# Performance work log

Hardware: AMD Instinct MI355X
Metric: run time of the kernel (lower is better)

## Reference

```python
import jax, jax.numpy as jnp
import numpy as np

N = 16384          # nodes
E_R = 524288       # radial edges (avg degree 32)
E_B = 32768        # bonded edges
N_TYPES = 20       # atom types
CS = 64            # scalar (0e) channels
CV = 32            # vector (1o) channels
EA = 16            # edge_attr_dim
EA_B = EA // 2     # bondedness embedding dim
EA_R = (EA + 1) // 2  # radial basis dim
CUTOFF = 1.5       # effective_radial_cutoff
L = 2              # n_layers
NORM = float(np.sqrt((E_R + E_B) / N))  # ~sqrt(avg degree) message normalization


def setup_inputs() -> dict:
    key = jax.random.key(0)
    ks = jax.random.split(key, 32)
    def rn(i, shape, scale=1.0):
        return jax.random.normal(ks[i], shape, dtype=jnp.float32) * scale
    s_e = 1.0 / np.sqrt(EA)
    inp = {}
    inp["pos"] = rn(0, (N, 3))
    inp["c_noise"] = rn(1, (1,))
    inp["atom_types"] = jax.random.randint(ks[2], (N,), 0, N_TYPES)
    inp["radial_edge_index"] = jax.random.randint(ks[3], (2, E_R), 0, N)
    inp["bonded_edge_index"] = jax.random.randint(ks[4], (2, E_B), 0, N)
    # learned parameters
    inp["atom_tab"] = rn(5, (N_TYPES, CS))
    inp["bond_tab"] = rn(6, (2, EA_B))
    inp["ns0_w"] = rn(7, (CS,), 0.1)
    inp["We0"] = rn(8, (EA, CS), s_e)
    inp["We1"] = rn(9, (EA, CS), s_e)
    inp["Wself0"] = rn(10, (CS, CS), 1.0 / np.sqrt(CS))
    inp["Ws0"] = rn(11, (CS, CS), 1.0 / np.sqrt(CS))
    inp["Wv0"] = rn(12, (CS, CV), 1.0 / np.sqrt(CS))
    inp["ns_w"] = rn(13, (L, CS + CV), 0.1)
    inp["We_ss"] = rn(14, (L, EA, CS), s_e)
    inp["We_vs"] = rn(15, (L, EA, CV), s_e)
    inp["We_sv"] = rn(16, (L, EA, CS), s_e)
    inp["We_vv"] = rn(17, (L, EA, CV), s_e)
    inp["We_vx"] = rn(18, (L, EA, CV), s_e)
    inp["Wmix_s"] = rn(19, (L, CS + CV, CS), 1.0 / np.sqrt(CS + CV))
    inp["Wmix_v"] = rn(20, (L, CS + 2 * CV, CV), 1.0 / np.sqrt(CS + 2 * CV))
    inp["Wself_s"] = rn(21, (L, CS, CS), 1.0 / np.sqrt(CS))
    inp["Wself_v"] = rn(22, (L, CV, CV), 1.0 / np.sqrt(CV))
    inp["skip_w"] = rn(23, (L, 2 * (CS + CV)), 0.1)
    inp["skip_b"] = rn(24, (L, 2 * (CS + CV)), 0.1)
    inp["w_out"] = rn(25, (CV,), 1.0 / np.sqrt(CV))
    inp["gain"] = jnp.asarray(0.5, dtype=jnp.float32)
    return inp


def _radial_basis(d):
    # e3nn soft_one_hot_linspace, basis='gaussian', cutoff=True
    centers = jnp.linspace(0.0, CUTOFF, EA_R + 2)[1:-1]
    step = centers[1] - centers[0]
    diff = (d[:, None] - centers[None, :]) / step
    return jnp.exp(-diff * diff) * 1.12


def reference(pos, c_noise, atom_tab, bond_tab, ns0_w, We0, We1, Wself0, Ws0, Wv0,
              ns_w, We_ss, We_vs, We_sv, We_vv, We_vx, Wmix_s, Wmix_v, Wself_s, Wself_v,
              skip_w, skip_b, w_out, gain, atom_types, radial_edge_index, bonded_edge_index):
    edge_index = jnp.concatenate([radial_edge_index, bonded_edge_index], axis=1)
    bond_mask = jnp.concatenate([jnp.zeros((E_R,), jnp.int32), jnp.ones((E_B,), jnp.int32)])
    src, dst = edge_index[0], edge_index[1]
    edge_vec = pos[src] - pos[dst]                      # [E,3]
    d = jnp.sqrt(jnp.sum(edge_vec * edge_vec, -1) + 1e-12)
    Y1 = jnp.sqrt(3.0) * edge_vec / d[:, None]          # l=1 SH, component norm; Y0 == 1
    edge_attr = jnp.concatenate([bond_tab[bond_mask], _radial_basis(d)], axis=-1)  # [E,EA]

    # atom embedding + initial noise-conditional scaling
    s = atom_tab[atom_types] * (1.0 + c_noise * ns0_w)  # [N,CS]

    # initial projector: scalar-input equivariant conv -> hidden irreps
    w0 = edge_attr @ We0
    w1 = edge_attr @ We1
    s_src = s[src]
    a_s = jax.ops.segment_sum(w0 * s_src, dst, num_segments=N) / NORM
    a_v = jax.ops.segment_sum((w1 * s_src)[:, :, None] * Y1[:, None, :], dst, num_segments=N) / NORM
    s_h = a_s @ Ws0 + s @ Wself0                        # [N,CS]
    v_h = jnp.einsum('nci,cd->ndi', a_v, Wv0)           # [N,CV,3]

    for l in range(L):
        # noise-conditional scaling (per-irrep-channel scalar scale)
        scale = 1.0 + c_noise * ns_w[l]
        ss = s_h * scale[:CS]
        vv = v_h * scale[CS:][None, :, None]
        ss_e = ss[src]
        vv_e = vv[src]
        # edge-attr-conditioned tensor-product weights
        w_ss = edge_attr @ We_ss[l]
        w_vs = edge_attr @ We_vs[l]
        w_sv = edge_attr @ We_sv[l]
        w_vv = edge_attr @ We_vv[l]
        w_vx = edge_attr @ We_vx[l]
        # CG tensor-product messages: 0x0->0, 1x1->0 (dot), 0x1->1, 1x0->1, 1x1->1 (cross)
        vdot = jnp.einsum('eci,ei->ec', vv_e, Y1)
        m_s = jnp.concatenate([w_ss * ss_e, w_vs * vdot], axis=-1)          # [E,CS+CV]
        m_v = jnp.concatenate([
            (w_sv * ss_e)[:, :, None] * Y1[:, None, :],
            w_vv[:, :, None] * vv_e,
            w_vx[:, :, None] * jnp.cross(vv_e, Y1[:, None, :]),
        ], axis=1)                                                          # [E,CS+2CV,3]
        a_s = jax.ops.segment_sum(m_s, dst, num_segments=N) / NORM
        a_v = jax.ops.segment_sum(m_v, dst, num_segments=N) / NORM
        new_s = a_s @ Wmix_s[l] + ss @ Wself_s[l]
        new_v = jnp.einsum('nci,cd->ndi', a_v, Wmix_v[l]) + jnp.einsum('nci,cd->ndi', vv, Wself_v[l])
        # noise-conditional skip connection (gated residual)
        g = jax.nn.sigmoid(skip_b[l] + c_noise * skip_w[l])
        s_h = g[:CS] * s_h + g[CS:2 * CS] * new_s
        g_v = g[2 * CS:]
        v_h = g_v[:CV][None, :, None] * v_h + g_v[CV:][None, :, None] * new_v

    # output head: 1o vectors -> 3D displacement, times output gain
    return jnp.einsum('nci,c->ni', v_h, w_out) * gain
```

## Files before the change

kernel.cpp:

```cpp
#include <hip/hip_runtime.h>
#include <math.h>

#define NA 16384
#define ER 524288
#define EB 32768
#define ET 557056
#define INV_NORM 0.17149858514250882f
#define SQRT3 1.7320508075688772f
#define RB_STEP (1.5f/9.0f)
#define BINS 512
#define DMAX 2.5f
#define INV_H ((float)BINS / DMAX)
#define TBL_ELEMS (2 * BINS * 256)

__device__ __forceinline__ float sigmoidf_(float x) { return 1.f / (1.f + __expf(-x)); }

__device__ __forceinline__ int edge_dst(int e, const int* __restrict__ rad, const int* __restrict__ bon) {
  return (e < ER) ? rad[ER + e] : bon[EB + (e - ER)];
}

__global__ void k_zero(int* __restrict__ count) {
  count[blockIdx.x * 256 + threadIdx.x] = 0;
}

__global__ void k_hist(const int* __restrict__ rad, const int* __restrict__ bon, int* __restrict__ count) {
  int e = blockIdx.x * 256 + threadIdx.x;
  atomicAdd(&count[edge_dst(e, rad, bon)], 1);
}

__global__ void k_scan(int* __restrict__ count, int* __restrict__ offsets) {
  __shared__ int part[256];
  int t = threadIdx.x;
  int base = t * 64;
  int s = 0;
  for (int j = 0; j < 64; ++j) s += count[base + j];
  part[t] = s;
  __syncthreads();
  for (int off = 1; off < 256; off <<= 1) {
    int v = (t >= off) ? part[t - off] : 0;
    __syncthreads();
    part[t] += v;
    __syncthreads();
  }
  int run = part[t] - s;
  for (int j = 0; j < 64; ++j) {
    int c = count[base + j];
    offsets[base + j] = run;
    count[base + j] = run;
    run += c;
  }
  if (t == 255) offsets[NA] = run;
}

__global__ void k_fill(const int* __restrict__ rad, const int* __restrict__ bon,
                       int* __restrict__ cursor, int* __restrict__ sorted) {
  int e = blockIdx.x * 256 + threadIdx.x;
  int d = edge_dst(e, rad, bon);
  int slot = atomicAdd(&cursor[d], 1);
  sorted[slot] = e;
}

__global__ void k_edge_pre(const float* __restrict__ pos,
                           const int* __restrict__ rad, const int* __restrict__ bon,
                           const int* __restrict__ sorted, float* __restrict__ rec8) {
  int idx = blockIdx.x * 256 + threadIdx.x;
  int e = sorted[idx];
  int src, dst, v;
  if (e < ER) { src = rad[e]; dst = rad[ER + e]; v = 0; }
  else        { src = bon[e - ER]; dst = bon[EB + e - ER]; v = 1; }
  float dx = pos[src * 3] - pos[dst * 3];
  float dy = pos[src * 3 + 1] - pos[dst * 3 + 1];
  float dz = pos[src * 3 + 2] - pos[dst * 3 + 2];
  float dist = sqrtf(dx * dx + dy * dy + dz * dz + 1e-12f);
  float inv = 1.f / dist;
  float fq = fminf(dist * INV_H, BINS - 1.001f);
  int q = (int)fq;
  float frac = fq - (float)q;
  int qoff = (v * BINS + q) << 8;
  float* rp = rec8 + (size_t)idx * 8;
  *(float4*)rp = make_float4(__int_as_float(src), SQRT3 * dx * inv, SQRT3 * dy * inv, SQRT3 * dz * inv);
  rp[4] = frac;
  rp[5] = __int_as_float(qoff);
}

__global__ void k_build(const float* __restrict__ We0, const float* __restrict__ We1,
                        const float* __restrict__ We_ss, const float* __restrict__ We_vs,
                        const float* __restrict__ We_sv, const float* __restrict__ We_vv,
                        const float* __restrict__ We_vx, const float* __restrict__ bond_tab,
                        float* __restrict__ tabs) {
  int q = blockIdx.x, t = blockIdx.y, v = blockIdx.z, c = threadIdx.x;
  float d0 = q * (DMAX / BINS), d1 = (q + 1) * (DMAX / BINS);
  float rb0[8], rb1[8];
#pragma unroll
  for (int k = 0; k < 8; ++k) {
    float f0 = (d0 - (k + 1) * RB_STEP) * (1.f / RB_STEP);
    float f1 = (d1 - (k + 1) * RB_STEP) * (1.f / RB_STEP);
    rb0[k] = 1.12f * __expf(-f0 * f0);
    rb1[k] = 1.12f * __expf(-f1 * f1);
  }
  const float* A;
  const float* B;
  int stride, coff;
  bool hasB = true;
  if (t == 0) { A = We0; B = We1; stride = 64; coff = c; }
  else if (t == 1 || t == 3) {
    int l = (t == 3);
    A = We_ss + l * 1024; B = We_sv + l * 1024; stride = 64; coff = c;
  } else {
    int l = (t == 4);
    stride = 32; coff = c & 31;
    if (c < 32) { A = We_vs + l * 512; B = We_vv + l * 512; }
    else        { A = We_vx + l * 512; B = nullptr; hasB = false; }
  }
  float ba = 0, bb = 0, a0 = 0, a1 = 0, b0 = 0, b1 = 0;
#pragma unroll
  for (int k = 0; k < 8; ++k) {
    float bt = bond_tab[v * 8 + k];
    float av_lo = A[k * stride + coff], av_hi = A[(8 + k) * stride + coff];
    ba += bt * av_lo;
    a0 += rb0[k] * av_hi; a1 += rb1[k] * av_hi;
    if (hasB) {
      float bv_lo = B[k * stride + coff], bv_hi = B[(8 + k) * stride + coff];
      bb += bt * bv_lo;
      b0 += rb0[k] * bv_hi; b1 += rb1[k] * bv_hi;
    }
  }
  float* o = tabs + (size_t)t * TBL_ELEMS + (((size_t)v * BINS + q) << 8) + c * 4;
  o[0] = ba + a0; o[1] = a1 - a0; o[2] = bb + b0; o[3] = b1 - b0;
}

__global__ void k_embed(const float* __restrict__ atom_tab, const int* __restrict__ types,
                        const float* __restrict__ ns0_w, const float* __restrict__ cnoise,
                        float* __restrict__ s_feat) {
  int tid = blockIdx.x * 256 + threadIdx.x;
  int n = tid >> 6, c = tid & 63;
  float cn = cnoise[0];
  s_feat[tid] = atom_tab[types[n] * 64 + c] * (1.f + cn * ns0_w[c]);
}

__global__ __launch_bounds__(256, 6) void k_agg0(
    const int* __restrict__ offsets, const float* __restrict__ rec8,
    const float* __restrict__ T0, const float* __restrict__ s_feat,
    float* __restrict__ a_s, float* __restrict__ a_v) {
  int lane = threadIdx.x & 63;
  int n = blockIdx.x * 4 + (threadIdx.x >> 6);
  float acc = 0, a0 = 0, a1 = 0, a2 = 0;
  int beg = __builtin_amdgcn_readfirstlane(offsets[n]);
  int end = __builtin_amdgcn_readfirstlane(offsets[n + 1]);
  if (beg < end) {
    const float* rp0 = rec8 + (size_t)beg * 8;
    float4 rA = *(const float4*)rp0;
    float2 rB = *(const float2*)(rp0 + 4);
    int i1 = beg + (beg + 1 < end ? 1 : 0);
    const float* rp1 = rec8 + (size_t)i1 * 8;
    float4 nA = *(const float4*)rp1;
    float2 nB = *(const float2*)(rp1 + 4);
    float4 t4 = *(const float4*)(T0 + __float_as_int(rB.y) + (lane << 2));
    float sv = s_feat[((size_t)__float_as_int(rA.x) << 6) + lane];
#pragma unroll 2
    for (int idx = beg; idx < end; ++idx) {
      float4 pt4 = *(const float4*)(T0 + __float_as_int(nB.y) + (lane << 2));
      float psv = s_feat[((size_t)__float_as_int(nA.x) << 6) + lane];
      int i2 = (idx + 2 < end) ? idx + 2 : end - 1;
      const float* rp2 = rec8 + (size_t)i2 * 8;
      float4 fA = *(const float4*)rp2;
      float2 fB = *(const float2*)(rp2 + 4);
      float frac = rB.x;
      float w0 = fmaf(frac, t4.y, t4.x);
      float w1 = fmaf(frac, t4.w, t4.z);
      acc += w0 * sv;
      float t = w1 * sv;
      a0 += t * rA.y; a1 += t * rA.z; a2 += t * rA.w;
      rA = nA; rB = nB; nA = fA; nB = fB; t4 = pt4; sv = psv;
    }
  }
  a_s[n * 64 + lane] = acc * INV_NORM;
  *(float4*)(a_v + ((size_t)n << 8) + (lane << 2)) =
      make_float4(a0 * INV_NORM, a1 * INV_NORM, a2 * INV_NORM, 0.f);
}

__global__ __launch_bounds__(256, 6) void k_agg_layer(
    const float* __restrict__ cnoise, const float* __restrict__ nsw,
    const int* __restrict__ offsets, const float* __restrict__ rec8,
    const float* __restrict__ TS, const float* __restrict__ TU,
    const float* __restrict__ sh_in, const float* __restrict__ vh_in,
    float* __restrict__ a_s, float* __restrict__ a_v) {
  int lane = threadIdx.x & 63;
  int n = blockIdx.x * 4 + (threadIdx.x >> 6);
  int vc = lane & 31;
  bool low = lane < 32;
  float cn = cnoise[0];
  float scale_s = 1.f + cn * nsw[lane];
  float scale_v = 1.f + cn * nsw[64 + vc];

  float ms = 0;
  float av0 = 0, av1 = 0, av2 = 0;
  float ms2 = 0;
  float b0 = 0, b1 = 0, b2 = 0;
  int beg = __builtin_amdgcn_readfirstlane(offsets[n]);
  int end = __builtin_amdgcn_readfirstlane(offsets[n + 1]);
  if (beg < end) {
    const float* rp0 = rec8 + (size_t)beg * 8;
    float4 rA = *(const float4*)rp0;
    float2 rB = *(const float2*)(rp0 + 4);
    int i1 = beg + (beg + 1 < end ? 1 : 0);
    const float* rp1 = rec8 + (size_t)i1 * 8;
    float4 nA = *(const float4*)rp1;
    float2 nB = *(const float2*)(rp1 + 4);
    int src0 = __float_as_int(rA.x);
    int qo0 = __float_as_int(rB.y);
    float4 s4 = *(const float4*)(TS + qo0 + (lane << 2));
    float4 u4 = *(const float4*)(TU + qo0 + (lane << 2));
    float ss = sh_in[((size_t)src0 << 6) + lane];
    float4 v4 = *(const float4*)(vh_in + ((size_t)src0 << 7) + (vc << 2));
#pragma unroll 2
    for (int idx = beg; idx < end; ++idx) {
      int nsrc = __float_as_int(nA.x);
      int nqo = __float_as_int(nB.y);
      float4 ps4 = *(const float4*)(TS + nqo + (lane << 2));
      float4 pu4 = *(const float4*)(TU + nqo + (lane << 2));
      float pss = sh_in[((size_t)nsrc << 6) + lane];
      float4 pv4 = *(const float4*)(vh_in + ((size_t)nsrc << 7) + (vc << 2));
      int i2 = (idx + 2 < end) ? idx + 2 : end - 1;
      const float* rp2 = rec8 + (size_t)i2 * 8;
      float4 fA = *(const float4*)rp2;
      float2 fB = *(const float2*)(rp2 + 4);
      float frac = rB.x;
      float y0 = rA.y, y1 = rA.z, y2 = rA.w;
      float wS  = fmaf(frac, s4.y, s4.x);
      float wSV = fmaf(frac, s4.w, s4.z);
      float wA  = fmaf(frac, u4.y, u4.x);
      float wB  = fmaf(frac, u4.w, u4.z);
      float v0 = v4.x, v1 = v4.y, v2 = v4.z;
      ms += wS * ss;
      float t = wSV * ss;
      av0 += t * y0; av1 += t * y1; av2 += t * y2;
      float vdot = v0 * y0 + v1 * y1 + v2 * y2;
      ms2 += wA * vdot;
      float cx = v1 * y2 - v2 * y1;
      float cy = v2 * y0 - v0 * y2;
      float cz = v0 * y1 - v1 * y0;
      float m0 = low ? v0 : cx;
      float m1 = low ? v1 : cy;
      float m2 = low ? v2 : cz;
      float wM = low ? wB : wA;
      b0 += wM * m0; b1 += wM * m1; b2 += wM * m2;
      rA = nA; rB = nB; nA = fA; nB = fB;
      s4 = ps4; u4 = pu4; ss = pss; v4 = pv4;
    }
  }
  float fs = scale_s * INV_NORM;
  float fv = scale_v * INV_NORM;
  a_s[n * 96 + lane] = ms * fs;
  float* avn = a_v + ((size_t)n << 9);
  *(float4*)(avn + (lane << 2)) = make_float4(av0 * fs, av1 * fs, av2 * fs, 0.f);
  if (low) {
    a_s[n * 96 + 64 + vc] = ms2 * fv;
    *(float4*)(avn + ((64 + vc) << 2)) = make_float4(b0 * fv, b1 * fv, b2 * fv, 0.f);
  } else {
    *(float4*)(avn + ((96 + vc) << 2)) = make_float4(b0 * fv, b1 * fv, b2 * fv, 0.f);
  }
}

__global__ __launch_bounds__(256, 4) void k_init_s(
    const float* __restrict__ a_s, const float* __restrict__ s_feat,
    const float* __restrict__ Ws0, const float* __restrict__ Wself0,
    float* __restrict__ sh) {
  __shared__ float W1[64 * 64];
  __shared__ float W2[64 * 64];
  __shared__ float La[8 * 64];
  __shared__ float Lf[8 * 64];
  int tid = threadIdx.x;
  for (int i = tid; i < 1024; i += 256) {
    ((float4*)W1)[i] = ((const float4*)Ws0)[i];
    ((float4*)W2)[i] = ((const float4*)Wself0)[i];
  }
  int base = blockIdx.x * 8;
  for (int i = tid; i < 512; i += 256) {
    La[i] = a_s[(size_t)base * 64 + i];
    Lf[i] = s_feat[(size_t)base * 64 + i];
  }
  __syncthreads();
  int d = tid & 63, g = tid >> 6;
  int n0 = base + g * 2;
  const float* A0 = La + g * 128;
  const float* A1 = A0 + 64;
  const float* F0 = Lf + g * 128;
  const float* F1 = F0 + 64;
  float a0 = 0, a1 = 0;
#pragma unroll 8
  for (int c = 0; c < 64; ++c) {
    float w1 = W1[c * 64 + d], w2 = W2[c * 64 + d];
    a0 += A0[c] * w1 + F0[c] * w2;
    a1 += A1[c] * w1 + F1[c] * w2;
  }
  sh[(size_t)n0 * 64 + d] = a0;
  sh[(size_t)(n0 + 1) * 64 + d] = a1;
}

__global__ __launch_bounds__(256, 4) void k_init_v(
    const float* __restrict__ a_v, const float* __restrict__ Wv0,
    float* __restrict__ vh) {
  __shared__ float W[64 * 32];
  int tid = threadIdx.x;
  for (int i = tid; i < 512; i += 256) ((float4*)W)[i] = ((const float4*)Wv0)[i];
  __syncthreads();
  int d = tid & 31, g = tid >> 5;
  int n = blockIdx.x * 8 + g;
  const float4* av = (const float4*)(a_v + ((size_t)n << 8));
  float x = 0, y = 0, z = 0;
#pragma unroll 4
  for (int c = 0; c < 64; ++c) {
    float4 a = av[c];
    float w = W[c * 32 + d];
    x += a.x * w; y += a.y * w; z += a.z * w;
  }
  *(float4*)(vh + ((size_t)n << 7) + (d << 2)) = make_float4(x, y, z, 0.f);
}

__global__ __launch_bounds__(256, 4) void k_mix_s(
    const float* __restrict__ a_s, const float* __restrict__ sh_in,
    const float* __restrict__ Wmix_s, const float* __restrict__ Wself_s,
    const float* __restrict__ nsw, const float* __restrict__ skw,
    const float* __restrict__ skb, const float* __restrict__ cnoise,
    float* __restrict__ sh_out) {
  __shared__ float Wm[96 * 64];
  __shared__ float Wsf[64 * 64];
  __shared__ float La[8 * 96];
  int tid = threadIdx.x;
  float cn = cnoise[0];
  for (int i = tid; i < 96 * 16; i += 256) ((float4*)Wm)[i] = ((const float4*)Wmix_s)[i];
  for (int i = tid; i < 64 * 16; i += 256) {
    float4 wv = ((const float4*)Wself_s)[i];
    int c = i >> 4;
    float sc = 1.f + cn * nsw[c];
    wv.x *= sc; wv.y *= sc; wv.z *= sc; wv.w *= sc;
    ((float4*)Wsf)[i] = wv;
  }
  int base = blockIdx.x * 8;
  for (int i = tid; i < 8 * 96; i += 256) La[i] = a_s[(size_t)base * 96 + i];
  __syncthreads();
  int d = tid & 63, g = tid >> 6;
  int n0 = base + g * 2;
  const float* A0 = La + (g * 2) * 96;
  const float* A1 = A0 + 96;
  const float* s0p = sh_in + (size_t)n0 * 64;
  const float* s1p = s0p + 64;
  float acc0 = 0, acc1 = 0;
#pragma unroll 8
  for (int c = 0; c < 96; ++c) {
    float w = Wm[c * 64 + d];
    acc0 += A0[c] * w;
    acc1 += A1[c] * w;
  }
#pragma unroll 8
  for (int c = 0; c < 64; ++c) {
    float w = Wsf[c * 64 + d];
    acc0 += s0p[c] * w;
    acc1 += s1p[c] * w;
  }
  float g1 = sigmoidf_(skb[d] + cn * skw[d]);
  float g2 = sigmoidf_(skb[64 + d] + cn * skw[64 + d]);
  sh_out[(size_t)n0 * 64 + d] = g1 * s0p[d] + g2 * acc0;
  sh_out[(size_t)(n0 + 1) * 64 + d] = g1 * s1p[d] + g2 * acc1;
}

__global__ __launch_bounds__(256, 4) void k_mix_v(
    const float* __restrict__ a_v, const float* __restrict__ vh_in,
    const float* __restrict__ Wmix_v, const float* __restrict__ Wself_v,
    const float* __restrict__ nsw, const float* __restrict__ skw,
    const float* __restrict__ skb, const float* __restrict__ cnoise,
    float* __restrict__ vh_out) {
  __shared__ float Wm[128 * 32];
  __shared__ float Wsf[32 * 32];
  int tid = threadIdx.x;
  float cn = cnoise[0];
  for (int i = tid; i < 128 * 8; i += 256) ((float4*)Wm)[i] = ((const float4*)Wmix_v)[i];
  for (int i = tid; i < 32 * 8; i += 256) {
    float4 wv = ((const float4*)Wself_v)[i];
    int c = i >> 3;
    float sc = 1.f + cn * nsw[64 + c];
    wv.x *= sc; wv.y *= sc; wv.z *= sc; wv.w *= sc;
    ((float4*)Wsf)[i] = wv;
  }
  __syncthreads();
  int d = tid & 31, g = tid >> 5;
  int n = blockIdx.x * 8 + g;
  const float4* av = (const float4*)(a_v + ((size_t)n << 9));
  const float4* vr = (const float4*)(vh_in + ((size_t)n << 7));
  float x = 0, y = 0, z = 0;
#pragma unroll 4
  for (int c = 0; c < 128; ++c) {
    float4 a = av[c];
    float w = Wm[c * 32 + d];
    x += a.x * w; y += a.y * w; z += a.z * w;
  }
#pragma unroll 4
  for (int c = 0; c < 32; ++c) {
    float4 vv = vr[c];
    float w = Wsf[c * 32 + d];
    x += vv.x * w; y += vv.y * w; z += vv.z * w;
  }
  float g3 = sigmoidf_(skb[128 + d] + cn * skw[128 + d]);
  float g4 = sigmoidf_(skb[160 + d] + cn * skw[160 + d]);
  float4 vi = vr[d];
  *(float4*)(vh_out + ((size_t)n << 7) + (d << 2)) =
      make_float4(g3 * vi.x + g4 * x, g3 * vi.y + g4 * y, g3 * vi.z + g4 * z, 0.f);
}

__global__ void k_out(const float* __restrict__ vh, const float* __restrict__ w_out,
                      const float* __restrict__ gain, float* __restrict__ out) {
  int tid = blockIdx.x * 256 + threadIdx.x;
  int n = tid / 3, i = tid - n * 3;
  float acc = 0;
  for (int c = 0; c < 32; ++c) acc += vh[((size_t)n << 7) + c * 4 + i] * w_out[c];
  out[tid] = acc * gain[0];
}

extern "C" void kernel_launch(void* const* d_in, const int* in_sizes, int n_in,
                              void* d_out, int out_size, void* d_ws, size_t ws_size,
                              hipStream_t stream) {
  (void)in_sizes; (void)n_in; (void)out_size; (void)ws_size;
  const float* pos     = (const float*)d_in[0];
  const float* cn      = (const float*)d_in[1];
  const int*   types   = (const int*)d_in[2];
  const int*   rad     = (const int*)d_in[3];
  const int*   bon     = (const int*)d_in[4];
  const float* atom_tab= (const float*)d_in[5];
  const float* bond_tab= (const float*)d_in[6];
  const float* ns0_w   = (const float*)d_in[7];
  const float* We0     = (const float*)d_in[8];
  const float* We1     = (const float*)d_in[9];
  const float* Wself0  = (const float*)d_in[10];
  const float* Ws0     = (const float*)d_in[11];
  const float* Wv0     = (const float*)d_in[12];
  const float* ns_w    = (const float*)d_in[13];
  const float* We_ss   = (const float*)d_in[14];
  const float* We_vs   = (const float*)d_in[15];
  const float* We_sv   = (const float*)d_in[16];
  const float* We_vv   = (const float*)d_in[17];
  const float* We_vx   = (const float*)d_in[18];
  const float* Wmix_s  = (const float*)d_in[19];
  const float* Wmix_v  = (const float*)d_in[20];
  const float* Wself_s = (const float*)d_in[21];
  const float* Wself_v = (const float*)d_in[22];
  const float* skip_w  = (const float*)d_in[23];
  const float* skip_b  = (const float*)d_in[24];
  const float* w_out   = (const float*)d_in[25];
  const float* gain    = (const float*)d_in[26];

  char* ws = (char*)d_ws;
  size_t o = 0;
  auto alloc = [&](size_t bytes) -> void* {
    void* p = ws + o;
    o += (bytes + 255) & ~(size_t)255;
    return p;
  };
  float* s_feat = (float*)alloc((size_t)NA * 64 * 4);
  float* a_s    = (float*)alloc((size_t)NA * 96 * 4);
  float* a_v    = (float*)alloc((size_t)NA * 512 * 4);
  float* sh0    = (float*)alloc((size_t)NA * 64 * 4);
  float* sh1    = (float*)alloc((size_t)NA * 64 * 4);
  float* vh0    = (float*)alloc((size_t)NA * 128 * 4);
  float* vh1    = (float*)alloc((size_t)NA * 128 * 4);
  int* count    = (int*)alloc((size_t)NA * 4);
  int* offsets  = (int*)alloc((size_t)(NA + 1) * 4);
  int* sorted   = (int*)alloc((size_t)ET * 4);
  float* rec8   = (float*)alloc((size_t)ET * 32);
  float* tabs   = (float*)alloc((size_t)5 * TBL_ELEMS * 4);
  float* shb[2] = {sh0, sh1};
  float* vhb[2] = {vh0, vh1};

  k_zero<<<NA / 256, 256, 0, stream>>>(count);
  k_hist<<<ET / 256, 256, 0, stream>>>(rad, bon, count);
  k_scan<<<1, 256, 0, stream>>>(count, offsets);
  k_fill<<<ET / 256, 256, 0, stream>>>(rad, bon, count, sorted);
  k_edge_pre<<<ET / 256, 256, 0, stream>>>(pos, rad, bon, sorted, rec8);
  k_build<<<dim3(BINS, 5, 2), 64, 0, stream>>>(We0, We1, We_ss, We_vs, We_sv, We_vv, We_vx,
                                               bond_tab, tabs);

  k_embed<<<NA * 64 / 256, 256, 0, stream>>>(atom_tab, types, ns0_w, cn, s_feat);
  k_agg0<<<NA / 4, 256, 0, stream>>>(offsets, rec8, tabs, s_feat, a_s, a_v);
  k_init_s<<<NA / 8, 256, 0, stream>>>(a_s, s_feat, Ws0, Wself0, shb[0]);
  k_init_v<<<NA / 8, 256, 0, stream>>>(a_v, Wv0, vhb[0]);

  for (int l = 0; l < 2; ++l) {
    int bin = l & 1, bout = 1 - bin;
    const float* TS = tabs + (size_t)(1 + 2 * l) * TBL_ELEMS;
    const float* TU = tabs + (size_t)(2 + 2 * l) * TBL_ELEMS;
    k_agg_layer<<<NA / 4, 256, 0, stream>>>(
        cn, ns_w + l * 96, offsets, rec8, TS, TU, shb[bin], vhb[bin], a_s, a_v);
    k_mix_s<<<NA / 8, 256, 0, stream>>>(
        a_s, shb[bin], Wmix_s + l * 96 * 64, Wself_s + l * 64 * 64,
        ns_w + l * 96, skip_w + l * 192, skip_b + l * 192, cn, shb[bout]);
    k_mix_v<<<NA / 8, 256, 0, stream>>>(
        a_v, vhb[bin], Wmix_v + l * 128 * 32, Wself_v + l * 32 * 32,
        ns_w + l * 96, skip_w + l * 192, skip_b + l * 192, cn, vhb[bout]);
  }
  k_out<<<NA * 3 / 256, 256, 0, stream>>>(vhb[0], w_out, gain, (float*)d_out);
}
```

Before: 537.0 us.

## Store edge-weight tables and gathered node features in bf16 for aggregation

Packs the per-bin interpolation tables into bf16 pairs, halving table size, and adds bf16 shadow copies of scalar and vector node features. The aggregation kernels gather these instead of fp32. Gathered bytes per edge drop by about half, at the cost of extra bf16 writes in the producing kernels and reduced precision in the messages. The single-block scan is also split into a three-kernel multi-block scan.

```diff
diff --git a/kernel.cpp b/kernel.cpp
--- a/kernel.cpp
+++ b/kernel.cpp
@@ -11,9 +11,23 @@
 #define BINS 512
 #define DMAX 2.5f
 #define INV_H ((float)BINS / DMAX)
-#define TBL_ELEMS (2 * BINS * 256)
+#define TBLU (2 * BINS * 128)
+
+typedef unsigned int uint32;
+typedef unsigned short ushort16;
 
 __device__ __forceinline__ float sigmoidf_(float x) { return 1.f / (1.f + __expf(-x)); }
+
+__device__ __forceinline__ ushort16 f2bf(float x) {
+  uint32 u = __float_as_uint(x);
+  u = u + 0x7FFFu + ((u >> 16) & 1u);
+  return (ushort16)(u >> 16);
+}
+__device__ __forceinline__ uint32 packbf(float hi, float lo) {
+  return ((uint32)f2bf(hi) << 16) | (uint32)f2bf(lo);
+}
+__device__ __forceinline__ float bfhi(uint32 u) { return __uint_as_float(u & 0xFFFF0000u); }
+__device__ __forceinline__ float bflo(uint32 u) { return __uint_as_float(u << 16); }
 
 __device__ __forceinline__ int edge_dst(int e, const int* __restrict__ rad, const int* __restrict__ bon) {
   return (e < ER) ? rad[ER + e] : bon[EB + (e - ER)];
@@ -28,28 +42,40 @@
   atomicAdd(&count[edge_dst(e, rad, bon)], 1);
 }
 
-__global__ void k_scan(int* __restrict__ count, int* __restrict__ offsets) {
-  __shared__ int part[256];
-  int t = threadIdx.x;
-  int base = t * 64;
-  int s = 0;
-  for (int j = 0; j < 64; ++j) s += count[base + j];
-  part[t] = s;
+__global__ void k_scan1(const int* __restrict__ count, int* __restrict__ partial) {
+  __shared__ int red[256];
+  int b = blockIdx.x, t = threadIdx.x;
+  red[t] = count[b * 256 + t];
+  __syncthreads();
+  for (int s = 128; s > 0; s >>= 1) {
+    if (t < s) red[t] += red[t + s];
+    __syncthreads();
+  }
+  if (t == 0) partial[b] = red[0];
+}
+
+__global__ void k_scan2(int* __restrict__ partial) {
+  int run = 0;
+  for (int i = 0; i < 64; ++i) { int c = partial[i]; partial[i] = run; run += c; }
+}
+
+__global__ void k_scan3(const int* __restrict__ count, const int* __restrict__ partial,
+                        int* __restrict__ offsets, int* __restrict__ cursor) {
+  __shared__ int sc[256];
+  int b = blockIdx.x, t = threadIdx.x;
+  int v = count[b * 256 + t];
+  sc[t] = v;
   __syncthreads();
   for (int off = 1; off < 256; off <<= 1) {
-    int v = (t >= off) ? part[t - off] : 0;
+    int x = (t >= off) ? sc[t - off] : 0;
     __syncthreads();
-    part[t] += v;
+    sc[t] += x;
     __syncthreads();
   }
-  int run = part[t] - s;
-  for (int j = 0; j < 64; ++j) {
-    int c = count[base + j];
-    offsets[base + j] = run;
-    count[base + j] = run;
-    run += c;
-  }
-  if (t == 255) offsets[NA] = run;
+  int excl = sc[t] - v + partial[b];
+  offsets[b * 256 + t] = excl;
+  cursor[b * 256 + t] = excl;
+  if (b == 63 && t == 255) offsets[NA] = excl + v;
 }
 
 __global__ void k_fill(const int* __restrict__ rad, const int* __restrict__ bon,
@@ -76,7 +102,7 @@
   float fq = fminf(dist * INV_H, BINS - 1.001f);
   int q = (int)fq;
   float frac = fq - (float)q;
-  int qoff = (v * BINS + q) << 8;
+  int qoff = (v * BINS + q) << 7;
   float* rp = rec8 + (size_t)idx * 8;
   *(float4*)rp = make_float4(__int_as_float(src), SQRT3 * dx * inv, SQRT3 * dy * inv, SQRT3 * dz * inv);
   rp[4] = frac;
@@ -87,7 +113,7 @@
                         const float* __restrict__ We_ss, const float* __restrict__ We_vs,
                         const float* __restrict__ We_sv, const float* __restrict__ We_vv,
                         const float* __restrict__ We_vx, const float* __restrict__ bond_tab,
-                        float* __restrict__ tabs) {
+                        uint32* __restrict__ tabs) {
   int q = blockIdx.x, t = blockIdx.y, v = blockIdx.z, c = threadIdx.x;
   float d0 = q * (DMAX / BINS), d1 = (q + 1) * (DMAX / BINS);
   float rb0[8], rb1[8];
@@ -125,22 +151,25 @@
       b0 += rb0[k] * bv_hi; b1 += rb1[k] * bv_hi;
     }
   }
-  float* o = tabs + (size_t)t * TBL_ELEMS + (((size_t)v * BINS + q) << 8) + c * 4;
-  o[0] = ba + a0; o[1] = a1 - a0; o[2] = bb + b0; o[3] = b1 - b0;
+  uint32* o = tabs + (size_t)t * TBLU + (((size_t)v * BINS + q) << 7) + c * 2;
+  o[0] = packbf(ba + a0, a1 - a0);
+  o[1] = hasB ? packbf(bb + b0, b1 - b0) : 0u;
 }
 
 __global__ void k_embed(const float* __restrict__ atom_tab, const int* __restrict__ types,
                         const float* __restrict__ ns0_w, const float* __restrict__ cnoise,
-                        float* __restrict__ s_feat) {
+                        float* __restrict__ s_feat, ushort16* __restrict__ s_bf) {
   int tid = blockIdx.x * 256 + threadIdx.x;
   int n = tid >> 6, c = tid & 63;
   float cn = cnoise[0];
-  s_feat[tid] = atom_tab[types[n] * 64 + c] * (1.f + cn * ns0_w[c]);
+  float v = atom_tab[types[n] * 64 + c] * (1.f + cn * ns0_w[c]);
+  s_feat[tid] = v;
+  s_bf[tid] = f2bf(v);
 }
 
 __global__ __launch_bounds__(256, 6) void k_agg0(
     const int* __restrict__ offsets, const float* __restrict__ rec8,
-    const float* __restrict__ T0, const float* __restrict__ s_feat,
+    const uint32* __restrict__ T0, const ushort16* __restrict__ s_bf,
     float* __restrict__ a_s, float* __restrict__ a_v) {
   int lane = threadIdx.x & 63;
   int n = blockIdx.x * 4 + (threadIdx.x >> 6);
@@ -155,23 +184,24 @@
     const float* rp1 = rec8 + (size_t)i1 * 8;
     float4 nA = *(const float4*)rp1;
     float2 nB = *(const float2*)(rp1 + 4);
-    float4 t4 = *(const float4*)(T0 + __float_as_int(rB.y) + (lane << 2));
-    float sv = s_feat[((size_t)__float_as_int(rA.x) << 6) + lane];
+    uint2 t2 = *(const uint2*)(T0 + __float_as_int(rB.y) + (lane << 1));
+    ushort16 su = s_bf[((size_t)__float_as_int(rA.x) << 6) + lane];
 #pragma unroll 2
     for (int idx = beg; idx < end; ++idx) {
-      float4 pt4 = *(const float4*)(T0 + __float_as_int(nB.y) + (lane << 2));
-      float psv = s_feat[((size_t)__float_as_int(nA.x) << 6) + lane];
+      uint2 pt2 = *(const uint2*)(T0 + __float_as_int(nB.y) + (lane << 1));
+      ushort16 psu = s_bf[((size_t)__float_as_int(nA.x) << 6) + lane];
       int i2 = (idx + 2 < end) ? idx + 2 : end - 1;
       const float* rp2 = rec8 + (size_t)i2 * 8;
       float4 fA = *(const float4*)rp2;
       float2 fB = *(const float2*)(rp2 + 4);
       float frac = rB.x;
-      float w0 = fmaf(frac, t4.y, t4.x);
-      float w1 = fmaf(frac, t4.w, t4.z);
+      float w0 = fmaf(frac, bflo(t2.x), bfhi(t2.x));
+      float w1 = fmaf(frac, bflo(t2.y), bfhi(t2.y));
+      float sv = __uint_as_float((uint32)su << 16);
       acc += w0 * sv;
       float t = w1 * sv;
       a0 += t * rA.y; a1 += t * rA.z; a2 += t * rA.w;
-      rA = nA; rB = nB; nA = fA; nB = fB; t4 = pt4; sv = psv;
+      rA = nA; rB = nB; nA = fA; nB = fB; t2 = pt2; su = psu;
     }
   }
   a_s[n * 64 + lane] = acc * INV_NORM;
@@ -182,8 +212,8 @@
 __global__ __launch_bounds__(256, 6) void k_agg_layer(
     const float* __restrict__ cnoise, const float* __restrict__ nsw,
     const int* __restrict__ offsets, const float* __restrict__ rec8,
-    const float* __restrict__ TS, const float* __restrict__ TU,
-    const float* __restrict__ sh_in, const float* __restrict__ vh_in,
+    const uint32* __restrict__ TS, const uint32* __restrict__ TU,
+    const ushort16* __restrict__ sh_bf, const uint32* __restrict__ vh_bf,
     float* __restrict__ a_s, float* __restrict__ a_v) {
   int lane = threadIdx.x & 63;
   int n = blockIdx.x * 4 + (threadIdx.x >> 6);
@@ -209,29 +239,30 @@
     float2 nB = *(const float2*)(rp1 + 4);
     int src0 = __float_as_int(rA.x);
     int qo0 = __float_as_int(rB.y);
-    float4 s4 = *(const float4*)(TS + qo0 + (lane << 2));
-    float4 u4 = *(const float4*)(TU + qo0 + (lane << 2));
-    float ss = sh_in[((size_t)src0 << 6) + lane];
-    float4 v4 = *(const float4*)(vh_in + ((size_t)src0 << 7) + (vc << 2));
+    uint2 tS = *(const uint2*)(TS + qo0 + (lane << 1));
+    uint2 tU = *(const uint2*)(TU + qo0 + (lane << 1));
+    ushort16 su = sh_bf[((size_t)src0 << 6) + lane];
+    uint2 vv = *(const uint2*)(vh_bf + ((size_t)src0 << 6) + (vc << 1));
 #pragma unroll 2
     for (int idx = beg; idx < end; ++idx) {
       int nsrc = __float_as_int(nA.x);
       int nqo = __float_as_int(nB.y);
-      float4 ps4 = *(const float4*)(TS + nqo + (lane << 2));
-      float4 pu4 = *(const float4*)(TU + nqo + (lane << 2));
-      float pss = sh_in[((size_t)nsrc << 6) + lane];
-      float4 pv4 = *(const float4*)(vh_in + ((size_t)nsrc << 7) + (vc << 2));
+      uint2 ptS = *(const uint2*)(TS + nqo + (lane << 1));
+      uint2 ptU = *(const uint2*)(TU + nqo + (lane << 1));
+      ushort16 psu = sh_bf[((size_t)nsrc << 6) + lane];
+      uint2 pvv = *(const uint2*)(vh_bf + ((size_t)nsrc << 6) + (vc << 1));
       int i2 = (idx + 2 < end) ? idx + 2 : end - 1;
       const float* rp2 = rec8 + (size_t)i2 * 8;
       float4 fA = *(const float4*)rp2;
       float2 fB = *(const float2*)(rp2 + 4);
       float frac = rB.x;
       float y0 = rA.y, y1 = rA.z, y2 = rA.w;
-      float wS  = fmaf(frac, s4.y, s4.x);
-      float wSV = fmaf(frac, s4.w, s4.z);
-      float wA  = fmaf(frac, u4.y, u4.x);
-      float wB  = fmaf(frac, u4.w, u4.z);
-      float v0 = v4.x, v1 = v4.y, v2 = v4.z;
+      float wS  = fmaf(frac, bflo(tS.x), bfhi(tS.x));
+      float wSV = fmaf(frac, bflo(tS.y), bfhi(tS.y));
+      float wA  = fmaf(frac, bflo(tU.x), bfhi(tU.x));
+      float wB  = fmaf(frac, bflo(tU.y), bfhi(tU.y));
+      float ss = __uint_as_float((uint32)su << 16);
+      float v0 = bfhi(vv.x), v1 = bflo(vv.x), v2 = bfhi(vv.y);
       ms += wS * ss;
       float t = wSV * ss;
       av0 += t * y0; av1 += t * y1; av2 += t * y2;
@@ -246,7 +277,7 @@
       float wM = low ? wB : wA;
       b0 += wM * m0; b1 += wM * m1; b2 += wM * m2;
       rA = nA; rB = nB; nA = fA; nB = fB;
-      s4 = ps4; u4 = pu4; ss = pss; v4 = pv4;
+      tS = ptS; tU = ptU; su = psu; vv = pvv;
     }
   }
   float fs = scale_s * INV_NORM;
@@ -265,7 +296,7 @@
 __global__ __launch_bounds__(256, 4) void k_init_s(
     const float* __restrict__ a_s, const float* __restrict__ s_feat,
     const float* __restrict__ Ws0, const float* __restrict__ Wself0,
-    float* __restrict__ sh) {
+    float* __restrict__ sh, ushort16* __restrict__ sh_bf) {
   __shared__ float W1[64 * 64];
   __shared__ float W2[64 * 64];
   __shared__ float La[8 * 64];
@@ -296,11 +327,13 @@
   }
   sh[(size_t)n0 * 64 + d] = a0;
   sh[(size_t)(n0 + 1) * 64 + d] = a1;
+  sh_bf[(size_t)n0 * 64 + d] = f2bf(a0);
+  sh_bf[(size_t)(n0 + 1) * 64 + d] = f2bf(a1);
 }
 
 __global__ __launch_bounds__(256, 4) void k_init_v(
     const float* __restrict__ a_v, const float* __restrict__ Wv0,
-    float* __restrict__ vh) {
+    float* __restrict__ vh, uint32* __restrict__ vh_bf) {
   __shared__ float W[64 * 32];
   int tid = threadIdx.x;
   for (int i = tid; i < 512; i += 256) ((float4*)W)[i] = ((const float4*)Wv0)[i];
@@ -316,6 +349,7 @@
     x += a.x * w; y += a.y * w; z += a.z * w;
   }
   *(float4*)(vh + ((size_t)n << 7) + (d << 2)) = make_float4(x, y, z, 0.f);
+  *(uint2*)(vh_bf + ((size_t)n << 6) + (d << 1)) = make_uint2(packbf(x, y), packbf(z, 0.f));
 }
 
 __global__ __launch_bounds__(256, 4) void k_mix_s(
@@ -323,7 +357,7 @@
     const float* __restrict__ Wmix_s, const float* __restrict__ Wself_s,
     const float* __restrict__ nsw, const float* __restrict__ skw,
     const float* __restrict__ skb, const float* __restrict__ cnoise,
-    float* __restrict__ sh_out) {
+    float* __restrict__ sh_out, ushort16* __restrict__ sh_bf_out) {
   __shared__ float Wm[96 * 64];
   __shared__ float Wsf[64 * 64];
   __shared__ float La[8 * 96];
@@ -361,8 +395,12 @@
   }
   float g1 = sigmoidf_(skb[d] + cn * skw[d]);
   float g2 = sigmoidf_(skb[64 + d] + cn * skw[64 + d]);
-  sh_out[(size_t)n0 * 64 + d] = g1 * s0p[d] + g2 * acc0;
-  sh_out[(size_t)(n0 + 1) * 64 + d] = g1 * s1p[d] + g2 * acc1;
+  float o0 = g1 * s0p[d] + g2 * acc0;
+  float o1 = g1 * s1p[d] + g2 * acc1;
+  sh_out[(size_t)n0 * 64 + d] = o0;
+  sh_out[(size_t)(n0 + 1) * 64 + d] = o1;
+  sh_bf_out[(size_t)n0 * 64 + d] = f2bf(o0);
+  sh_bf_out[(size_t)(n0 + 1) * 64 + d] = f2bf(o1);
 }
 
 __global__ __launch_bounds__(256, 4) void k_mix_v(
@@ -370,7 +408,7 @@
     const float* __restrict__ Wmix_v, const float* __restrict__ Wself_v,
     const float* __restrict__ nsw, const float* __restrict__ skw,
     const float* __restrict__ skb, const float* __restrict__ cnoise,
-    float* __restrict__ vh_out) {
+    float* __restrict__ vh_out, uint32* __restrict__ vh_bf_out) {
   __shared__ float Wm[128 * 32];
   __shared__ float Wsf[32 * 32];
   int tid = threadIdx.x;
@@ -404,8 +442,11 @@
   float g3 = sigmoidf_(skb[128 + d] + cn * skw[128 + d]);
   float g4 = sigmoidf_(skb[160 + d] + cn * skw[160 + d]);
   float4 vi = vr[d];
-  *(float4*)(vh_out + ((size_t)n << 7) + (d << 2)) =
-      make_float4(g3 * vi.x + g4 * x, g3 * vi.y + g4 * y, g3 * vi.z + g4 * z, 0.f);
+  float ox = g3 * vi.x + g4 * x;
+  float oy = g3 * vi.y + g4 * y;
+  float oz = g3 * vi.z + g4 * z;
+  *(float4*)(vh_out + ((size_t)n << 7) + (d << 2)) = make_float4(ox, oy, oz, 0.f);
+  *(uint2*)(vh_bf_out + ((size_t)n << 6) + (d << 1)) = make_uint2(packbf(ox, oy), packbf(oz, 0.f));
 }
 
 __global__ void k_out(const float* __restrict__ vh, const float* __restrict__ w_out,
@@ -456,46 +497,57 @@
     o += (bytes + 255) & ~(size_t)255;
     return p;
   };
-  float* s_feat = (float*)alloc((size_t)NA * 64 * 4);
-  float* a_s    = (float*)alloc((size_t)NA * 96 * 4);
-  float* a_v    = (float*)alloc((size_t)NA * 512 * 4);
-  float* sh0    = (float*)alloc((size_t)NA * 64 * 4);
-  float* sh1    = (float*)alloc((size_t)NA * 64 * 4);
-  float* vh0    = (float*)alloc((size_t)NA * 128 * 4);
-  float* vh1    = (float*)alloc((size_t)NA * 128 * 4);
-  int* count    = (int*)alloc((size_t)NA * 4);
-  int* offsets  = (int*)alloc((size_t)(NA + 1) * 4);
-  int* sorted   = (int*)alloc((size_t)ET * 4);
-  float* rec8   = (float*)alloc((size_t)ET * 32);
-  float* tabs   = (float*)alloc((size_t)5 * TBL_ELEMS * 4);
-  float* shb[2] = {sh0, sh1};
-  float* vhb[2] = {vh0, vh1};
+  float* s_feat  = (float*)alloc((size_t)NA * 64 * 4);
+  ushort16* s_bf = (ushort16*)alloc((size_t)NA * 64 * 2);
+  float* a_s     = (float*)alloc((size_t)NA * 96 * 4);
+  float* a_v     = (float*)alloc((size_t)NA * 512 * 4);
+  float* sh0     = (float*)alloc((size_t)NA * 64 * 4);
+  float* sh1     = (float*)alloc((size_t)NA * 64 * 4);
+  ushort16* shbf0= (ushort16*)alloc((size_t)NA * 64 * 2);
+  ushort16* shbf1= (ushort16*)alloc((size_t)NA * 64 * 2);
+  float* vh0     = (float*)alloc((size_t)NA * 128 * 4);
+  float* vh1     = (float*)alloc((size_t)NA * 128 * 4);
+  uint32* vhbf0  = (uint32*)alloc((size_t)NA * 64 * 4);
+  uint32* vhbf1  = (uint32*)alloc((size_t)NA * 64 * 4);
+  int* count     = (int*)alloc((size_t)NA * 4);
+  int* partial   = (int*)alloc((size_t)64 * 4);
+  int* offsets   = (int*)alloc((size_t)(NA + 1) * 4);
+  int* cursor    = (int*)alloc((size_t)NA * 4);
+  int* sorted    = (int*)alloc((size_t)ET * 4);
+  float* rec8    = (float*)alloc((size_t)ET * 32);
+  uint32* tabs   = (uint32*)alloc((size_t)5 * TBLU * 4);
+  float* shb[2]  = {sh0, sh1};
+  ushort16* shbf[2] = {shbf0, shbf1};
+  float* vhb[2]  = {vh0, vh1};
+  uint32* vhbf[2]= {vhbf0, vhbf1};
 
   k_zero<<<NA / 256, 256, 0, stream>>>(count);
   k_hist<<<ET / 256, 256, 0, stream>>>(rad, bon, count);
-  k_scan<<<1, 256, 0, stream>>>(count, offsets);
-  k_fill<<<ET / 256, 256, 0, stream>>>(rad, bon, count, sorted);
+  k_scan1<<<64, 256, 0, stream>>>(count, partial);
+  k_scan2<<<1, 1, 0, stream>>>(partial);
+  k_scan3<<<64, 256, 0, stream>>>(count, partial, offsets, cursor);
+  k_fill<<<ET / 256, 256, 0, stream>>>(rad, bon, cursor, sorted);
   k_edge_pre<<<ET / 256, 256, 0, stream>>>(pos, rad, bon, sorted, rec8);
   k_build<<<dim3(BINS, 5, 2), 64, 0, stream>>>(We0, We1, We_ss, We_vs, We_sv, We_vv, We_vx,
                                                bond_tab, tabs);
 
-  k_embed<<<NA * 64 / 256, 256, 0, stream>>>(atom_tab, types, ns0_w, cn, s_feat);
-  k_agg0<<<NA / 4, 256, 0, stream>>>(offsets, rec8, tabs, s_feat, a_s, a_v);
-  k_init_s<<<NA / 8, 256, 0, stream>>>(a_s, s_feat, Ws0, Wself0, shb[0]);
-  k_init_v<<<NA / 8, 256, 0, stream>>>(a_v, Wv0, vhb[0]);
+  k_embed<<<NA * 64 / 256, 256, 0, stream>>>(atom_tab, types, ns0_w, cn, s_feat, s_bf);
+  k_agg0<<<NA / 4, 256, 0, stream>>>(offsets, rec8, tabs, s_bf, a_s, a_v);
+  k_init_s<<<NA / 8, 256, 0, stream>>>(a_s, s_feat, Ws0, Wself0, shb[0], shbf[0]);
+  k_init_v<<<NA / 8, 256, 0, stream>>>(a_v, Wv0, vhb[0], vhbf[0]);
 
   for (int l = 0; l < 2; ++l) {
     int bin = l & 1, bout = 1 - bin;
-    const float* TS = tabs + (size_t)(1 + 2 * l) * TBL_ELEMS;
-    const float* TU = tabs + (size_t)(2 + 2 * l) * TBL_ELEMS;
+    const uint32* TS = tabs + (size_t)(1 + 2 * l) * TBLU;
+    const uint32* TU = tabs + (size_t)(2 + 2 * l) * TBLU;
     k_agg_layer<<<NA / 4, 256, 0, stream>>>(
-        cn, ns_w + l * 96, offsets, rec8, TS, TU, shb[bin], vhb[bin], a_s, a_v);
+        cn, ns_w + l * 96, offsets, rec8, TS, TU, shbf[bin], vhbf[bin], a_s, a_v);
     k_mix_s<<<NA / 8, 256, 0, stream>>>(
         a_s, shb[bin], Wmix_s + l * 96 * 64, Wself_s + l * 64 * 64,
-        ns_w + l * 96, skip_w + l * 192, skip_b + l * 192, cn, shb[bout]);
+        ns_w + l * 96, skip_w + l * 192, skip_b + l * 192, cn, shb[bout], shbf[bout]);
     k_mix_v<<<NA / 8, 256, 0, stream>>>(
         a_v, vhb[bin], Wmix_v + l * 128 * 32, Wself_v + l * 32 * 32,
-        ns_w + l * 96, skip_w + l * 192, skip_b + l * 192, cn, vhb[bout]);
+        ns_w + l * 96, skip_w + l * 192, skip_b + l * 192, cn, vhb[bout], vhbf[bout]);
   }
   k_out<<<NA * 3 / 256, 256, 0, stream>>>(vhb[0], w_out, gain, (float*)d_out);
 }
```

Measured after the change: 526.8 us. Within noise of the previous version (-1.9%).
